# Optimization experiments

Measured on AMD Instinct MI355X. Metric: run time of the kernel, lower is better.

## Reference

```python
import jax, jax.numpy as jnp
import numpy as np

B, H, W, C = 4, 128, 128, 64
MODES, SCHMIDT = 16, 4


def setup_inputs() -> dict:
    key = jax.random.key(0)
    k1, k2, k3 = jax.random.split(key, 3)
    # glorot-like scale for (M, M, C, C, S) weights: fan over modes*modes*C
    w_scale = float(np.sqrt(2.0 / (MODES * MODES * C + MODES * MODES * C)))
    return {
        "x": jax.random.normal(k1, (B, H, W, C), dtype=jnp.float32),
        "weights_real": jax.random.normal(k2, (MODES, MODES, C, C, SCHMIDT), dtype=jnp.float32) * w_scale,
        "weights_imag": jax.random.normal(k3, (MODES, MODES, C, C, SCHMIDT), dtype=jnp.float32) * w_scale,
        "modes": MODES,
        "schmidt_rank": SCHMIDT,
    }


def reference(x, weights_real, weights_imag, modes, schmidt_rank):
    # x: [B, H, W, C] real
    b, h, w, c = x.shape
    # quantum_fourier_modes: spatial Fourier transform truncated to `modes` per dim
    x_ft = jnp.fft.fftn(x, axes=(1, 2))[:, :modes, :modes, :]  # [B, M, M, C] complex64
    weights = weights_real + 1j * weights_imag                 # [M, M, C, O, S]
    # 'b...nc,mncos->b...mos' with ellipsis = first mode axis (k)
    out_ft = jnp.einsum("bknc,mncos->bkmos", x_ft, weights)    # [B, M, M, O, S]
    # Schmidt-rank recombination: sum over schmidt axis (normalized)
    out_modes = out_ft.sum(axis=-1) / float(np.sqrt(schmidt_rank))  # [B, M, M, O]
    o = out_modes.shape[-1]
    # inverse quantum_fourier_modes: zero-pad low modes back to full grid, inverse FFT
    full = jnp.zeros((b, h, w, o), dtype=out_modes.dtype)
    full = full.at[:, :modes, :modes, :].set(out_modes)
    out = jnp.fft.ifftn(full, axes=(1, 2))
    return out.real
```

## Files before the change

kernel.cpp:

```cpp
#include <hip/hip_runtime.h>


static constexpr int BATCH = 4;

static constexpr size_t XFT_OFF = 0;
static constexpr size_t OM_OFF  = 131072;
static constexpr size_t BIG_OFF = 262144;

__device__ __forceinline__ void init_trig_lds(float2* twl) {
    if (threadIdx.x < 128) {
        float s, c;
        sincosf(6.283185307179586f * (float)threadIdx.x * 0.0078125f, &s, &c);
        twl[threadIdx.x] = make_float2(c, s);
    }
}

__global__ __launch_bounds__(256) void k_dft_w(const float* __restrict__ x,
                                               float2* __restrict__ tmp1) {
    __shared__ float4 xs[2048];
    __shared__ float2 twl[128];
    init_trig_lds(twl);
    const int bid = blockIdx.x;
    const float4* x4 = reinterpret_cast<const float4*>(x) + (size_t)bid * 2048;
    #pragma unroll
    for (int i = 0; i < 8; ++i) xs[threadIdx.x + 256 * i] = x4[threadIdx.x + 256 * i];
    __syncthreads();
    const int n  = threadIdx.x >> 4;
    const int c4 = threadIdx.x & 15;
    float4 ar = make_float4(0.f, 0.f, 0.f, 0.f);
    float4 ai = make_float4(0.f, 0.f, 0.f, 0.f);
    int t = 0;
    #pragma unroll 8
    for (int w = 0; w < 128; ++w) {
        const float4 v  = xs[w * 16 + c4];
        const float2 tw = twl[t];
        t = (t + n) & 127;
        ar.x += v.x * tw.x; ai.x -= v.x * tw.y;
        ar.y += v.y * tw.x; ai.y -= v.y * tw.y;
        ar.z += v.z * tw.x; ai.z -= v.z * tw.y;
        ar.w += v.w * tw.x; ai.w -= v.w * tw.y;
    }
    float4* o = reinterpret_cast<float4*>(tmp1 + ((size_t)bid * 16 + n) * 64 + c4 * 4);
    o[0] = make_float4(ar.x, ai.x, ar.y, ai.y);
    o[1] = make_float4(ar.z, ai.z, ar.w, ai.w);
}

__global__ __launch_bounds__(256) void k_dft_h(const float2* __restrict__ tmp1,
                                               float2* __restrict__ xft) {
    __shared__ float2 twl[128];
    init_trig_lds(twl);
    __syncthreads();
    const int tid = blockIdx.x * 256 + threadIdx.x;
    const int c = tid & 63;
    const int n = (tid >> 6) & 15;
    const int k = (tid >> 10) & 15;
    const int b = tid >> 14;
    const float2* src = tmp1 + (size_t)b * 131072 + n * 64 + c;
    float2 acc = make_float2(0.f, 0.f);
    int t = 0;
    #pragma unroll 8
    for (int h = 0; h < 128; ++h) {
        const float2 a  = src[(size_t)h * 1024];
        const float2 tw = twl[t];
        t = (t + k) & 127;
        acc.x += a.x * tw.x + a.y * tw.y;
        acc.y += a.y * tw.x - a.x * tw.y;
    }
    xft[(size_t)(b * 16 + k) * 1024 + n * 64 + c] = acc;
}

__global__ __launch_bounds__(256) void k_gemm(const float2* __restrict__ xft,
                                              const float* __restrict__ wr,
                                              const float* __restrict__ wi,
                                              float2* __restrict__ P) {
    __shared__ float2 As[64 * 66];
    __shared__ float2 Bs[64 * 34];
    const int bid  = blockIdx.x;
    const int noct = bid & 7;
    const int oh   = (bid >> 3) & 1;
    const int m    = bid >> 4;
    const int ci = threadIdx.x & 15;
    const int ri = threadIdx.x >> 4;
    float accr[4][2] = {}, acci[4][2] = {};
    for (int nn = 0; nn < 2; ++nn) {
        const int n = noct * 2 + nn;
        #pragma unroll
        for (int i = 0; i < 8; ++i) {
            const int idx = threadIdx.x + 256 * i;
            const int row = idx >> 5, k2 = idx & 31;
            const float4 q = *reinterpret_cast<const float4*>(
                &xft[(size_t)row * 1024 + n * 64 + 2 * k2]);
            As[(2 * k2) * 66 + row]     = make_float2(q.x, q.y);
            As[(2 * k2 + 1) * 66 + row] = make_float2(q.z, q.w);
        }
        #pragma unroll
        for (int i = 0; i < 8; ++i) {
            const int idx = threadIdx.x + 256 * i;
            const int cc = idx >> 5, oo = idx & 31;
            const size_t wb = ((size_t)((m * 16 + n) * 64 + cc) * 64 + oh * 32 + oo) * 4;
            const float4 r4 = *reinterpret_cast<const float4*>(wr + wb);
            const float4 i4 = *reinterpret_cast<const float4*>(wi + wb);
            Bs[cc * 34 + oo] = make_float2((r4.x + r4.y + r4.z + r4.w) * 0.5f,
                                           (i4.x + i4.y + i4.z + i4.w) * 0.5f);
        }
        __syncthreads();
        #pragma unroll 8
        for (int kk = 0; kk < 64; ++kk) {
            const float4 a01 = *reinterpret_cast<const float4*>(&As[kk * 66 + 4 * ri]);
            const float4 a23 = *reinterpret_cast<const float4*>(&As[kk * 66 + 4 * ri + 2]);
            const float4 bb  = *reinterpret_cast<const float4*>(&Bs[kk * 34 + 2 * ci]);
            const float arr[4] = {a01.x, a01.z, a23.x, a23.z};
            const float aii[4] = {a01.y, a01.w, a23.y, a23.w};
            #pragma unroll
            for (int r = 0; r < 4; ++r) {
                accr[r][0] += arr[r] * bb.x - aii[r] * bb.y;
                acci[r][0] += arr[r] * bb.y + aii[r] * bb.x;
                accr[r][1] += arr[r] * bb.z - aii[r] * bb.w;
                acci[r][1] += arr[r] * bb.w + aii[r] * bb.z;
            }
        }
        __syncthreads();
    }
    float2* Pb = P + (size_t)bid * 2048;
    #pragma unroll
    for (int r = 0; r < 4; ++r) {
        const int row = 4 * ri + r;
        *reinterpret_cast<float4*>(&Pb[row * 32 + 2 * ci]) =
            make_float4(accr[r][0], acci[r][0], accr[r][1], acci[r][1]);
    }
}

__global__ __launch_bounds__(256) void k_reduce(const float2* __restrict__ P,
                                                float2* __restrict__ om) {
    const int gtid = blockIdx.x * 256 + threadIdx.x;
    const int o   = gtid & 63;
    const int mm  = (gtid >> 6) & 15;
    const int row = gtid >> 10;
    const int oh = o >> 5, oo = o & 31;
    const float2* p = P + (size_t)((mm * 2 + oh) * 8) * 2048 + row * 32 + oo;
    float2 acc = make_float2(0.f, 0.f);
    #pragma unroll
    for (int nq = 0; nq < 8; ++nq) {
        const float2 v = p[(size_t)nq * 2048];
        acc.x += v.x; acc.y += v.y;
    }
    om[(size_t)row * 1024 + mm * 64 + o] = acc;
}

__global__ __launch_bounds__(256) void k_ifft_h(const float2* __restrict__ om,
                                                float2* __restrict__ u) {
    __shared__ float2 twl[128];
    init_trig_lds(twl);
    const int bid = blockIdx.x;
    const int hq = bid & 3;
    const int m  = (bid >> 2) & 15;
    const int b  = bid >> 6;
    const int o  = threadIdx.x & 63;
    const int hs = threadIdx.x >> 6;
    __syncthreads();
    float2 v[16];
    #pragma unroll
    for (int k = 0; k < 16; ++k)
        v[k] = om[(size_t)(b * 16 + k) * 1024 + m * 64 + o];
    #pragma unroll
    for (int i = 0; i < 8; ++i) {
        const int h = hq * 32 + hs * 8 + i;
        float re = 0.f, im = 0.f;
        int t = 0;
        #pragma unroll
        for (int k = 0; k < 16; ++k) {
            const float2 tw = twl[t];
            t = (t + h) & 127;
            re += v[k].x * tw.x - v[k].y * tw.y;
            im += v[k].x * tw.y + v[k].y * tw.x;
        }
        u[((size_t)(b * 128 + h) * 16 + m) * 64 + o] = make_float2(re, im);
    }
}

__global__ __launch_bounds__(256) void k_ifft_w(const float2* __restrict__ u,
                                                float* __restrict__ out) {
    __shared__ float2 twl[128];
    init_trig_lds(twl);
    const int bid = blockIdx.x;
    const int o4 = threadIdx.x & 15;
    const int wg = threadIdx.x >> 4;
    __syncthreads();
    const float2* ub = u + (size_t)bid * 1024 + o4 * 4;
    float2 v[16][4];
    #pragma unroll
    for (int mm = 0; mm < 16; ++mm) {
        const float4 q0 = *reinterpret_cast<const float4*>(ub + (size_t)mm * 64);
        const float4 q1 = *reinterpret_cast<const float4*>(ub + (size_t)mm * 64 + 2);
        v[mm][0] = make_float2(q0.x, q0.y);
        v[mm][1] = make_float2(q0.z, q0.w);
        v[mm][2] = make_float2(q1.x, q1.y);
        v[mm][3] = make_float2(q1.z, q1.w);
    }
    const float inv = 1.0f / 16384.0f;
    #pragma unroll
    for (int i = 0; i < 8; ++i) {
        const int w = wg * 8 + i;
        float4 acc = make_float4(0.f, 0.f, 0.f, 0.f);
        int t = 0;
        #pragma unroll
        for (int mm = 0; mm < 16; ++mm) {
            const float2 tw = twl[t];
            t = (t + w) & 127;
            acc.x += v[mm][0].x * tw.x - v[mm][0].y * tw.y;
            acc.y += v[mm][1].x * tw.x - v[mm][1].y * tw.y;
            acc.z += v[mm][2].x * tw.x - v[mm][2].y * tw.y;
            acc.w += v[mm][3].x * tw.x - v[mm][3].y * tw.y;
        }
        acc.x *= inv; acc.y *= inv; acc.z *= inv; acc.w *= inv;
        *reinterpret_cast<float4*>(out + ((size_t)bid * 128 + w) * 64 + o4 * 4) = acc;
    }
}

extern "C" void kernel_launch(void* const* d_in, const int* in_sizes, int n_in,
                              void* d_out, int out_size, void* d_ws, size_t ws_size,
                              hipStream_t stream) {
    const float* x  = (const float*)d_in[0];
    const float* wr = (const float*)d_in[1];
    const float* wi = (const float*)d_in[2];
    float* out = (float*)d_out;
    float* ws  = (float*)d_ws;

    float2* xft = (float2*)(ws + XFT_OFF);
    float2* om  = (float2*)(ws + OM_OFF);
    float2* big = (float2*)(ws + BIG_OFF);

    k_dft_w <<<BATCH * 128, 256, 0, stream>>>(x, big);
    k_dft_h <<<256, 256, 0, stream>>>(big, xft);
    k_gemm  <<<256, 256, 0, stream>>>(xft, wr, wi, big);
    k_reduce<<<256, 256, 0, stream>>>(big, om);
    k_ifft_h<<<256, 256, 0, stream>>>(om, big);
    k_ifft_w<<<BATCH * 128, 256, 0, stream>>>(big, out);
}
```

Baseline: 147.0 us.

## Fuse GEMM with n-reduction and merge inverse DFT passes into one kernel

Replaces the split-K GEMM plus separate reduce kernel with a GEMM that has each block own a slice of 4 output channels for one mode and accumulate over all n and c directly. It writes a transposed mode-major buffer so the inverse H-pass can read contiguous float4s. The two inverse-DFT kernels are fused so the intermediate u stays in LDS instead of round-tripping through global memory. This cuts the launch count from six to four and removes two global intermediates. The cost is that each GEMM thread does a long 1024-term serial dot product with only 256 blocks and reads xft straight from global memory, which may reduce arithmetic reuse compared with the tiled version.

```diff
diff --git a/kernel.cpp b/kernel.cpp
--- a/kernel.cpp
+++ b/kernel.cpp
@@ -3,9 +3,9 @@
 
 static constexpr int BATCH = 4;
 
-static constexpr size_t XFT_OFF = 0;
-static constexpr size_t OM_OFF  = 131072;
-static constexpr size_t BIG_OFF = 262144;
+static constexpr size_t TMP_OFF = 0;
+static constexpr size_t XFT_OFF = 1048576;
+static constexpr size_t OMT_OFF = 1179648;
 
 __device__ __forceinline__ void init_trig_lds(float2* twl) {
     if (threadIdx.x < 128) {
@@ -69,134 +69,69 @@
     xft[(size_t)(b * 16 + k) * 1024 + n * 64 + c] = acc;
 }
 
-__global__ __launch_bounds__(256) void k_gemm(const float2* __restrict__ xft,
-                                              const float* __restrict__ wr,
-                                              const float* __restrict__ wi,
-                                              float2* __restrict__ P) {
-    __shared__ float2 As[64 * 66];
-    __shared__ float2 Bs[64 * 34];
-    const int bid  = blockIdx.x;
-    const int noct = bid & 7;
-    const int oh   = (bid >> 3) & 1;
-    const int m    = bid >> 4;
-    const int ci = threadIdx.x & 15;
-    const int ri = threadIdx.x >> 4;
-    float accr[4][2] = {}, acci[4][2] = {};
-    for (int nn = 0; nn < 2; ++nn) {
-        const int n = noct * 2 + nn;
-        #pragma unroll
-        for (int i = 0; i < 8; ++i) {
-            const int idx = threadIdx.x + 256 * i;
-            const int row = idx >> 5, k2 = idx & 31;
-            const float4 q = *reinterpret_cast<const float4*>(
-                &xft[(size_t)row * 1024 + n * 64 + 2 * k2]);
-            As[(2 * k2) * 66 + row]     = make_float2(q.x, q.y);
-            As[(2 * k2 + 1) * 66 + row] = make_float2(q.z, q.w);
-        }
-        #pragma unroll
-        for (int i = 0; i < 8; ++i) {
-            const int idx = threadIdx.x + 256 * i;
-            const int cc = idx >> 5, oo = idx & 31;
-            const size_t wb = ((size_t)((m * 16 + n) * 64 + cc) * 64 + oh * 32 + oo) * 4;
-            const float4 r4 = *reinterpret_cast<const float4*>(wr + wb);
-            const float4 i4 = *reinterpret_cast<const float4*>(wi + wb);
-            Bs[cc * 34 + oo] = make_float2((r4.x + r4.y + r4.z + r4.w) * 0.5f,
-                                           (i4.x + i4.y + i4.z + i4.w) * 0.5f);
-        }
-        __syncthreads();
-        #pragma unroll 8
-        for (int kk = 0; kk < 64; ++kk) {
-            const float4 a01 = *reinterpret_cast<const float4*>(&As[kk * 66 + 4 * ri]);
-            const float4 a23 = *reinterpret_cast<const float4*>(&As[kk * 66 + 4 * ri + 2]);
-            const float4 bb  = *reinterpret_cast<const float4*>(&Bs[kk * 34 + 2 * ci]);
-            const float arr[4] = {a01.x, a01.z, a23.x, a23.z};
-            const float aii[4] = {a01.y, a01.w, a23.y, a23.w};
-            #pragma unroll
-            for (int r = 0; r < 4; ++r) {
-                accr[r][0] += arr[r] * bb.x - aii[r] * bb.y;
-                acci[r][0] += arr[r] * bb.y + aii[r] * bb.x;
-                accr[r][1] += arr[r] * bb.z - aii[r] * bb.w;
-                acci[r][1] += arr[r] * bb.w + aii[r] * bb.z;
-            }
-        }
-        __syncthreads();
+__global__ __launch_bounds__(256) void k_gemm2(const float2* __restrict__ xft,
+                                               const float* __restrict__ wr,
+                                               const float* __restrict__ wi,
+                                               float2* __restrict__ omT) {
+    __shared__ float2 Bs[4096];
+    const int oq = blockIdx.x & 15;
+    const int m  = blockIdx.x >> 4;
+    #pragma unroll
+    for (int i = 0; i < 16; ++i) {
+        const int idx = threadIdx.x + 256 * i;
+        const int nn = idx >> 8, cc = (idx >> 2) & 63, oo = idx & 3;
+        const size_t wb = ((size_t)((m * 16 + nn) * 64 + cc) * 64 + oq * 4 + oo) * 4;
+        const float4 r4 = *reinterpret_cast<const float4*>(wr + wb);
+        const float4 i4 = *reinterpret_cast<const float4*>(wi + wb);
+        Bs[idx] = make_float2((r4.x + r4.y + r4.z + r4.w) * 0.5f,
+                              (i4.x + i4.y + i4.z + i4.w) * 0.5f);
     }
-    float2* Pb = P + (size_t)bid * 2048;
-    #pragma unroll
-    for (int r = 0; r < 4; ++r) {
-        const int row = 4 * ri + r;
-        *reinterpret_cast<float4*>(&Pb[row * 32 + 2 * ci]) =
-            make_float4(accr[r][0], acci[r][0], accr[r][1], acci[r][1]);
+    __syncthreads();
+    const int ol = threadIdx.x & 3;
+    const int r  = threadIdx.x >> 2;
+    const float4* xr = reinterpret_cast<const float4*>(xft + (size_t)r * 1024);
+    float accx = 0.f, accy = 0.f;
+    #pragma unroll 8
+    for (int k2 = 0; k2 < 512; ++k2) {
+        const float4 a  = xr[k2];
+        const float2 b0 = Bs[8 * k2 + ol];
+        const float2 b1 = Bs[8 * k2 + 4 + ol];
+        accx += a.x * b0.x - a.y * b0.y + a.z * b1.x - a.w * b1.y;
+        accy += a.x * b0.y + a.y * b0.x + a.z * b1.y + a.w * b1.x;
     }
+    const int b = r >> 4, k = r & 15;
+    const int o = oq * 4 + ol;
+    omT[(((size_t)b * 16 + m) * 64 + o) * 16 + k] = make_float2(accx, accy);
 }
 
-__global__ __launch_bounds__(256) void k_reduce(const float2* __restrict__ P,
-                                                float2* __restrict__ om) {
-    const int gtid = blockIdx.x * 256 + threadIdx.x;
-    const int o   = gtid & 63;
-    const int mm  = (gtid >> 6) & 15;
-    const int row = gtid >> 10;
-    const int oh = o >> 5, oo = o & 31;
-    const float2* p = P + (size_t)((mm * 2 + oh) * 8) * 2048 + row * 32 + oo;
-    float2 acc = make_float2(0.f, 0.f);
-    #pragma unroll
-    for (int nq = 0; nq < 8; ++nq) {
-        const float2 v = p[(size_t)nq * 2048];
-        acc.x += v.x; acc.y += v.y;
-    }
-    om[(size_t)row * 1024 + mm * 64 + o] = acc;
-}
-
-__global__ __launch_bounds__(256) void k_ifft_h(const float2* __restrict__ om,
-                                                float2* __restrict__ u) {
+__global__ __launch_bounds__(256) void k_idft(const float2* __restrict__ omT,
+                                              float* __restrict__ out) {
+    __shared__ float2 u_s[1024];
     __shared__ float2 twl[128];
     init_trig_lds(twl);
     const int bid = blockIdx.x;
-    const int hq = bid & 3;
-    const int m  = (bid >> 2) & 15;
-    const int b  = bid >> 6;
-    const int o  = threadIdx.x & 63;
-    const int hs = threadIdx.x >> 6;
+    const int h = bid & 127, b = bid >> 7;
     __syncthreads();
-    float2 v[16];
     #pragma unroll
-    for (int k = 0; k < 16; ++k)
-        v[k] = om[(size_t)(b * 16 + k) * 1024 + m * 64 + o];
-    #pragma unroll
-    for (int i = 0; i < 8; ++i) {
-        const int h = hq * 32 + hs * 8 + i;
+    for (int i = 0; i < 4; ++i) {
+        const int e = threadIdx.x + 256 * i;
+        const float4* src = reinterpret_cast<const float4*>(
+            omT + (((size_t)b * 16 + (e >> 6)) * 64 + (e & 63)) * 16);
         float re = 0.f, im = 0.f;
         int t = 0;
         #pragma unroll
-        for (int k = 0; k < 16; ++k) {
-            const float2 tw = twl[t];
-            t = (t + h) & 127;
-            re += v[k].x * tw.x - v[k].y * tw.y;
-            im += v[k].x * tw.y + v[k].y * tw.x;
+        for (int k8 = 0; k8 < 8; ++k8) {
+            const float4 q = src[k8];
+            const float2 tw0 = twl[t]; t = (t + h) & 127;
+            const float2 tw1 = twl[t]; t = (t + h) & 127;
+            re += q.x * tw0.x - q.y * tw0.y + q.z * tw1.x - q.w * tw1.y;
+            im += q.x * tw0.y + q.y * tw0.x + q.z * tw1.y + q.w * tw1.x;
         }
-        u[((size_t)(b * 128 + h) * 16 + m) * 64 + o] = make_float2(re, im);
+        u_s[e] = make_float2(re, im);
     }
-}
-
-__global__ __launch_bounds__(256) void k_ifft_w(const float2* __restrict__ u,
-                                                float* __restrict__ out) {
-    __shared__ float2 twl[128];
-    init_trig_lds(twl);
-    const int bid = blockIdx.x;
+    __syncthreads();
     const int o4 = threadIdx.x & 15;
     const int wg = threadIdx.x >> 4;
-    __syncthreads();
-    const float2* ub = u + (size_t)bid * 1024 + o4 * 4;
-    float2 v[16][4];
-    #pragma unroll
-    for (int mm = 0; mm < 16; ++mm) {
-        const float4 q0 = *reinterpret_cast<const float4*>(ub + (size_t)mm * 64);
-        const float4 q1 = *reinterpret_cast<const float4*>(ub + (size_t)mm * 64 + 2);
-        v[mm][0] = make_float2(q0.x, q0.y);
-        v[mm][1] = make_float2(q0.z, q0.w);
-        v[mm][2] = make_float2(q1.x, q1.y);
-        v[mm][3] = make_float2(q1.z, q1.w);
-    }
     const float inv = 1.0f / 16384.0f;
     #pragma unroll
     for (int i = 0; i < 8; ++i) {
@@ -205,12 +140,14 @@
         int t = 0;
         #pragma unroll
         for (int mm = 0; mm < 16; ++mm) {
-            const float2 tw = twl[t];
+            const float2 tw  = twl[t];
             t = (t + w) & 127;
-            acc.x += v[mm][0].x * tw.x - v[mm][0].y * tw.y;
-            acc.y += v[mm][1].x * tw.x - v[mm][1].y * tw.y;
-            acc.z += v[mm][2].x * tw.x - v[mm][2].y * tw.y;
-            acc.w += v[mm][3].x * tw.x - v[mm][3].y * tw.y;
+            const float4 u01 = *reinterpret_cast<const float4*>(&u_s[mm * 64 + o4 * 4]);
+            const float4 u23 = *reinterpret_cast<const float4*>(&u_s[mm * 64 + o4 * 4 + 2]);
+            acc.x += u01.x * tw.x - u01.y * tw.y;
+            acc.y += u01.z * tw.x - u01.w * tw.y;
+            acc.z += u23.x * tw.x - u23.y * tw.y;
+            acc.w += u23.z * tw.x - u23.w * tw.y;
         }
         acc.x *= inv; acc.y *= inv; acc.z *= inv; acc.w *= inv;
         *reinterpret_cast<float4*>(out + ((size_t)bid * 128 + w) * 64 + o4 * 4) = acc;
@@ -226,14 +163,12 @@
     float* out = (float*)d_out;
     float* ws  = (float*)d_ws;
 
-    float2* xft = (float2*)(ws + XFT_OFF);
-    float2* om  = (float2*)(ws + OM_OFF);
-    float2* big = (float2*)(ws + BIG_OFF);
+    float2* tmp1 = (float2*)(ws + TMP_OFF);
+    float2* xft  = (float2*)(ws + XFT_OFF);
+    float2* omT  = (float2*)(ws + OMT_OFF);
 
-    k_dft_w <<<BATCH * 128, 256, 0, stream>>>(x, big);
-    k_dft_h <<<256, 256, 0, stream>>>(big, xft);
-    k_gemm  <<<256, 256, 0, stream>>>(xft, wr, wi, big);
-    k_reduce<<<256, 256, 0, stream>>>(big, om);
-    k_ifft_h<<<256, 256, 0, stream>>>(om, big);
-    k_ifft_w<<<BATCH * 128, 256, 0, stream>>>(big, out);
+    k_dft_w<<<BATCH * 128, 256, 0, stream>>>(x, tmp1);
+    k_dft_h<<<256, 256, 0, stream>>>(tmp1, xft);
+    k_gemm2<<<256, 256, 0, stream>>>(xft, wr, wi, omT);
+    k_idft <<<BATCH * 128, 256, 0, stream>>>(omT, out);
 }
```

Measured after the change: 168.3 us. +14.5%, slower.
